# Optimization experiments

Measured on AMD Instinct MI355X. Metric: run time of the kernel, lower is better.

## Reference

```python
import jax, jax.numpy as jnp
import numpy as np

E = 1024
H = 16
DH = E // H
EPS = 1e-8
GRAM_W = 1.5


def _gram_scores(q, k1, k2):
    # q: [BH, L, D], k1/k2: [BH, S, D] -> [BH, L, S]
    ll = jnp.sum(q * q, -1)[:, :, None]          # [BH, L, 1]
    vv = jnp.sum(k1 * k1, -1)[:, None, :]        # [BH, 1, S]
    aa = jnp.sum(k2 * k2, -1)[:, None, :]
    va = jnp.sum(k1 * k2, -1)[:, None, :]
    lv = jnp.einsum('bld,bsd->bls', q, k1)
    la = jnp.einsum('bld,bsd->bls', q, k2)
    det = ll * (vv * aa - va * va) - lv * (lv * aa - la * va) + la * (lv * va - la * vv)
    return -jnp.sqrt(jnp.clip(det, EPS, None))


def setup_inputs() -> dict:
    key = jax.random.key(0)
    ks = jax.random.split(key, 20)
    L, B, S = 512, 4, 1024
    inp = {
        'query': jax.random.normal(ks[0], (L, B, E), jnp.float32),
        'mod1': jax.random.normal(ks[1], (S, B, E), jnp.float32),
        'mod2': jax.random.normal(ks[2], (S, B, E), jnp.float32),
    }
    # Linear params stored as [in, out] (y = x @ W + b), 8 linears
    names = ['q', 'k1', 'k2', 'v1', 'v2', 'g1', 'g2', 'o']
    for i, n in enumerate(names):
        inp[n + '_w'] = jax.random.normal(ks[3 + 2 * i], (E, E), jnp.float32) * 0.02
        inp[n + '_b'] = jax.random.normal(ks[4 + 2 * i], (E,), jnp.float32) * 0.02
    return inp


def reference(query, mod1, mod2,
              q_w, q_b, k1_w, k1_b, k2_w, k2_b, v1_w, v1_b, v2_w, v2_b,
              g1_w, g1_b, g2_w, g2_b, o_w, o_b):
    L, B, _ = query.shape
    S = mod1.shape[0]
    scaling = DH ** -0.5

    def lin(x, w, b):
        return x @ w + b

    def split_heads(x, n):  # [n, B, E] -> [B*H, n, DH]
        return x.reshape(n, B * H, DH).transpose(1, 0, 2)

    q = split_heads(lin(query, q_w, q_b) * scaling, L)
    k1 = split_heads(lin(mod1, k1_w, k1_b), S)
    k2 = split_heads(lin(mod2, k2_w, k2_b), S)
    v1 = split_heads(lin(mod1, v1_w, v1_b), S)
    v2 = split_heads(lin(mod2, v2_w, v2_b), S)

    w1 = jnp.einsum('bld,bsd->bls', q, k1)
    w2 = jnp.einsum('bld,bsd->bls', q, k2)
    gram = _gram_scores(q, k1, k2)
    logits = GRAM_W * gram + w1 + w2          # [BH, L, S]
    attn = jax.nn.softmax(logits, axis=-1)

    def merge_heads(x):  # [B*H, L, DH] -> [L, B, E]
        return x.transpose(1, 0, 2).reshape(L, B, E)

    out1 = merge_heads(jnp.einsum('bls,bsd->bld', attn, v1))
    out2 = merge_heads(jnp.einsum('bls,bsd->bld', attn, v2))
    gate1 = jax.nn.sigmoid(lin(query, g1_w, g1_b))
    gate2 = jax.nn.sigmoid(lin(query, g2_w, g2_b))
    attn_output = lin((out1 * gate1 + out2 * gate2) / 2.0, o_w, o_b)
    avg_weights = attn.reshape(B, H, L, S).mean(axis=1)
    return attn_output, avg_weights
```

## Files before the change

### kernel.cpp

```cpp
#include <hip/hip_runtime.h>
#include <cstddef>
#include <cstdint>

typedef unsigned short ushort_t;
typedef unsigned int uint_t;
typedef __attribute__((ext_vector_type(8))) short short8;
typedef __attribute__((ext_vector_type(4))) float f32x4;

#define EDIM 1024
#define NHEAD 16
#define HDIM 64
#define NB 4
#define LQ 512
#define SK 1024
#define BHD 64

__device__ __forceinline__ ushort_t f2b(float f) {
    uint_t u = __float_as_uint(f);
    return (ushort_t)((u + 0x7fffu + ((u >> 16) & 1u)) >> 16);
}
__device__ __forceinline__ float b2f(ushort_t b) {
    return __uint_as_float(((uint_t)b) << 16);
}

__device__ __forceinline__ void gload_lds16(const void* g, void* l) {
    __builtin_amdgcn_global_load_lds((const __attribute__((address_space(1))) void*)g,
                                     (__attribute__((address_space(3))) void*)l, 16, 0, 0);
}

struct MegaArgs {
    const ushort_t *qx, *m1h, *m1l, *m2h, *m2l;
    const ushort_t *Wqg, *Wkv1, *Wkv2, *Wk1l, *Wk2l;
    const float *q_b, *k1_b, *k2_b, *v1_b, *v2_b, *g1_b, *g2_b;
    float *K1f, *K2f;
    ushort_t *V1b, *V2b, *Qb, *G1b, *G2b;
};

__global__ __launch_bounds__(256, 2)
void mega_gemm(MegaArgs a)
{
    __shared__ ushort_t As[128 * 64];
    __shared__ ushort_t Bs[128 * 64];
    const int tid = threadIdx.x;
    const int wave = tid >> 6, lane = tid & 63;
    const int ln = lane & 15, lq = lane >> 4;
    const int wm = wave & 1, wn = wave >> 1;
    const int cswz = (lane & 7) ^ ((lane >> 3) & 7);
    const int mrl = lane >> 3;

    const int id = blockIdx.x;
    const ushort_t *A, *Al, *B, *Bl;
    const float* bias;
    int npass, row0, col0, kind;
    if (id < 512) {
        kind = id >> 8;
        const int t = id & 255;
        col0 = (t & 7) * 128; row0 = (t >> 3) * 128; npass = 3;
        A = kind ? a.m2h : a.m1h;  Al = kind ? a.m2l : a.m1l;
        B = kind ? a.Wkv2 : a.Wkv1; Bl = kind ? a.Wk2l : a.Wk1l;
        bias = kind ? a.k2_b : a.k1_b;
    } else if (id < 1024) {
        int t = id - 512; kind = 2 + (t >> 8); t &= 255;
        col0 = (t & 7) * 128; row0 = (t >> 3) * 128; npass = 1;
        A = (kind == 2) ? a.m1h : a.m2h; Al = A;
        B = ((kind == 2) ? a.Wkv1 : a.Wkv2) + (size_t)1024 * 1024; Bl = B;
        bias = (kind == 2) ? a.v1_b : a.v2_b;
    } else {
        const int t = id - 1024; kind = 4;
        const int c = t % 24, rr = t / 24;
        col0 = c * 128; row0 = rr * 128; npass = 1;
        A = a.qx; Al = A; B = a.Wqg; Bl = B;
        const int seg = c >> 3;
        bias = (seg == 0) ? a.q_b : ((seg == 1) ? a.g1_b : a.g2_b);
    }

    f32x4 zero = {0.f, 0.f, 0.f, 0.f};
    f32x4 acc[4][4];
#pragma unroll
    for (int i = 0; i < 4; ++i)
#pragma unroll
        for (int j = 0; j < 4; ++j) acc[i][j] = zero;

    for (int pp = 0; pp < npass; ++pp) {
        const ushort_t* Ab = (pp == 2) ? Al : A;
        const ushort_t* Bb = (pp == 1) ? Bl : B;
        for (int kk = 0; kk < 1024; kk += 64) {
            __syncthreads();
#pragma unroll
            for (int j = 0; j < 4; ++j) {
                const int mr = (wave * 4 + j) * 8 + mrl;
                gload_lds16(Ab + (size_t)(row0 + mr) * 1024 + kk + cswz * 8,
                            (void*)(As + (wave * 4 + j) * 512));
                gload_lds16(Bb + (size_t)(col0 + mr) * 1024 + kk + cswz * 8,
                            (void*)(Bs + (wave * 4 + j) * 512));
            }
            __syncthreads();
#pragma unroll
            for (int sub = 0; sub < 2; ++sub) {
                short8 af[4], bfv[4];
#pragma unroll
                for (int i = 0; i < 4; ++i) {
                    const int ml = wm * 64 + i * 16 + ln;
                    af[i] = *(const short8*)(As + ml * 64 + (((sub * 4 + lq) ^ (ml & 7)) * 8));
                    const int nl = wn * 64 + i * 16 + ln;
                    bfv[i] = *(const short8*)(Bs + nl * 64 + (((sub * 4 + lq) ^ (nl & 7)) * 8));
                }
#pragma unroll
                for (int i = 0; i < 4; ++i)
#pragma unroll
                    for (int j = 0; j < 4; ++j)
                        acc[i][j] = __builtin_amdgcn_mfma_f32_16x16x32_bf16(af[i], bfv[j], acc[i][j], 0, 0, 0);
            }
        }
    }

#pragma unroll
    for (int i = 0; i < 4; ++i) {
#pragma unroll
        for (int r = 0; r < 4; ++r) {
            const int row = row0 + wm * 64 + i * 16 + lq * 4 + r;
#pragma unroll
            for (int j = 0; j < 4; ++j) {
                const int col = col0 + wn * 64 + j * 16 + ln;
                const int lc = col & 1023;
                float v = acc[i][j][r] + bias[lc];
                if (kind <= 1) {
                    const int s = row >> 2, b = row & 3, h = lc >> 6, d = lc & 63;
                    float* Y = kind ? a.K2f : a.K1f;
                    Y[(((size_t)(b * 16 + h)) * 1024 + s) * 64 + d] = v;
                } else if (kind <= 3) {
                    const int s = row >> 2, b = row & 3, h = lc >> 6, d = lc & 63;
                    ushort_t* Y = (kind == 2) ? a.V1b : a.V2b;
                    Y[(((size_t)(b * 16 + h)) * 1024 + s) * 64 + d] = f2b(v);
                } else {
                    const int seg = col >> 10;
                    if (seg == 0) {
                        v *= 0.125f;
                        const int s = row >> 2, b = row & 3, h = lc >> 6, d = lc & 63;
                        a.Qb[(((size_t)(b * 16 + h)) * 512 + s) * 64 + d] = f2b(v);
                    } else {
                        v = 1.0f / (1.0f + __expf(-v));
                        ushort_t* Y = (seg == 1) ? a.G1b : a.G2b;
                        Y[(size_t)row * 1024 + lc] = f2b(v);
                    }
                }
            }
        }
    }
}

struct CastArgs {
    const float* q; const float* m1; const float* m2;
    ushort_t* qx; ushort_t* m1h; ushort_t* m1l; ushort_t* m2h; ushort_t* m2l;
    const float* wsrc[8];
    ushort_t* whi[8];
    ushort_t* wlo[8];
};

__global__ __launch_bounds__(256)
void casts_kernel(CastArgs a)
{
    __shared__ float T[64][65];
    const int id = blockIdx.x;
    const int tid = threadIdx.x;
    if (id < 1024) {
        const size_t i = ((size_t)id * 256 + tid) * 8;
        float4 x = *(const float4*)(a.q + i);
        float4 y = *(const float4*)(a.q + i + 4);
        ushort_t o[8] = {f2b(x.x), f2b(x.y), f2b(x.z), f2b(x.w), f2b(y.x), f2b(y.y), f2b(y.z), f2b(y.w)};
        *(uint4*)( (void*)(a.qx + i) ) = *(const uint4*)o;
    } else if (id < 5120) {
        const int t = id - 1024;
        const int which = t >> 11;
        const float* x = which ? a.m2 : a.m1;
        ushort_t* yh = which ? a.m2h : a.m1h;
        ushort_t* yl = which ? a.m2l : a.m1l;
        const size_t i = ((size_t)(t & 2047) * 256 + tid) * 8;
        float v[8];
        *(float4*)v = *(const float4*)(x + i);
        *(float4*)(v + 4) = *(const float4*)(x + i + 4);
        ushort_t oh[8], ol[8];
#pragma unroll
        for (int k = 0; k < 8; ++k) {
            oh[k] = f2b(v[k]);
            ol[k] = f2b(v[k] - b2f(oh[k]));
        }
        *(uint4*)( (void*)(yh + i) ) = *(const uint4*)oh;
        *(uint4*)( (void*)(yl + i) ) = *(const uint4*)ol;
    } else {
        const int t = id - 5120;
        const int z = t >> 8, x = t & 15, y = (t >> 4) & 15;
        const float* W = a.wsrc[z];
        ushort_t* Th = a.whi[z];
        ushort_t* Tl = a.wlo[z];
        const int k0 = x * 64, n0 = y * 64;
        const int r = tid >> 2, cg = (tid & 3) * 16;
#pragma unroll
        for (int u = 0; u < 4; ++u) {
            float4 v = *(const float4*)(W + (size_t)(k0 + r) * 1024 + n0 + cg + u * 4);
            T[r][cg + u * 4 + 0] = v.x; T[r][cg + u * 4 + 1] = v.y;
            T[r][cg + u * 4 + 2] = v.z; T[r][cg + u * 4 + 3] = v.w;
        }
        __syncthreads();
        ushort_t oh[16], ol[16];
#pragma unroll
        for (int u = 0; u < 16; ++u) {
            float v = T[cg + u][r];
            oh[u] = f2b(v);
            ol[u] = f2b(v - b2f(oh[u]));
        }
        ushort_t* dh = Th + (size_t)(n0 + r) * 1024 + k0 + cg;
        *(uint4*)( (void*)dh ) = *(const uint4*)oh;
        *(uint4*)( (void*)(dh + 8) ) = *(const uint4*)(oh + 8);
        if (Tl) {
            ushort_t* dl = Tl + (size_t)(n0 + r) * 1024 + k0 + cg;
            *(uint4*)( (void*)dl ) = *(const uint4*)ol;
            *(uint4*)( (void*)(dl + 8) ) = *(const uint4*)(ol + 8);
        }
    }
}

__global__ __launch_bounds__(256)
void prep_kernel(const float* __restrict__ K1f, const float* __restrict__ K2f,
                 ushort_t* __restrict__ K1b, ushort_t* __restrict__ K2b,
                 float* __restrict__ vv, float* __restrict__ aa, float* __restrict__ va,
                 const ushort_t* __restrict__ Qb, float* __restrict__ ll,
                 const ushort_t* __restrict__ V1b, const ushort_t* __restrict__ V2b,
                 ushort_t* __restrict__ V1t, ushort_t* __restrict__ V2t)
{
    __shared__ float T[64][65];
    const int id = blockIdx.x;
    const int tid = threadIdx.x;
    const int wave = tid >> 6, lane = tid & 63;
    if (id < 16384) {
        const int row = id * 4 + wave;
        const float x1 = K1f[(size_t)row * 64 + lane];
        const float x2 = K2f[(size_t)row * 64 + lane];
        K1b[(size_t)row * 64 + lane] = f2b(x1);
        K2b[(size_t)row * 64 + lane] = f2b(x2);
        float s1 = x1 * x1, s2 = x2 * x2, s3 = x1 * x2;
#pragma unroll
        for (int o = 1; o < 64; o <<= 1) {
            s1 += __shfl_xor(s1, o);
            s2 += __shfl_xor(s2, o);
            s3 += __shfl_xor(s3, o);
        }
        if (lane == 0) { vv[row] = s1; aa[row] = s2; va[row] = s3; }
    } else if (id < 24576) {
        const int row = (id - 16384) * 4 + wave;
        const float x = b2f(Qb[(size_t)row * 64 + lane]);
        float s = x * x;
#pragma unroll
        for (int o = 1; o < 64; o <<= 1) s += __shfl_xor(s, o);
        if (lane == 0) ll[row] = s;
    } else {
        const int t = id - 24576;
        const int z = t >> 10, bh = (t >> 4) & 63, s0 = (t & 15) * 64;
        const ushort_t* S = z ? V2b : V1b;
        ushort_t* D = z ? V2t : V1t;
        const int r = tid >> 2, cg = (tid & 3) * 16;
        ushort_t buf[16];
        const ushort_t* sp = S + ((size_t)bh * 1024 + s0 + r) * 64 + cg;
        *(uint4*)buf = *(const uint4*)sp;
        *(uint4*)(buf + 8) = *(const uint4*)(sp + 8);
#pragma unroll
        for (int u = 0; u < 16; ++u) T[r][cg + u] = b2f(buf[u]);
        __syncthreads();
        ushort_t o[16];
#pragma unroll
        for (int u = 0; u < 16; ++u) o[u] = f2b(T[cg + u][r]);
        ushort_t* d = D + ((size_t)bh * 64 + r) * 1024 + s0 + cg;
        *(uint4*)( (void*)d ) = *(const uint4*)o;
        *(uint4*)( (void*)(d + 8) ) = *(const uint4*)(o + 8);
    }
}

__global__ __launch_bounds__(256, 2)
void scores_kernel(const ushort_t* __restrict__ Qb, const ushort_t* __restrict__ K1b,
                   const ushort_t* __restrict__ K2b, const float* __restrict__ ll,
                   const float* __restrict__ vv, const float* __restrict__ aa,
                   const float* __restrict__ va, float* __restrict__ logits)
{
    __shared__ ushort_t Qs[128 * 64];
    __shared__ ushort_t K1s[128 * 64];
    __shared__ ushort_t K2s[128 * 64];
    __shared__ float llS[128], vvS[128], aaS[128], vaS[128];
    const int tid = threadIdx.x;
    const int wave = tid >> 6, lane = tid & 63;
    const int ln = lane & 15, lq = lane >> 4;
    const int wm = wave & 1, wn = wave >> 1;
    const int bh = blockIdx.z;
    const int l0 = blockIdx.y * 128, s0 = blockIdx.x * 128;
    const int cswz = (lane & 7) ^ ((lane >> 3) & 7);
    const int mrl = lane >> 3;

    if (tid < 128) {
        llS[tid] = ll[(size_t)bh * 512 + l0 + tid];
        vvS[tid] = vv[(size_t)bh * 1024 + s0 + tid];
        aaS[tid] = aa[(size_t)bh * 1024 + s0 + tid];
        vaS[tid] = va[(size_t)bh * 1024 + s0 + tid];
    }
#pragma unroll
    for (int j = 0; j < 4; ++j) {
        const int mr = (wave * 4 + j) * 8 + mrl;
        gload_lds16(Qb + ((size_t)bh * 512 + l0 + mr) * 64 + cswz * 8, (void*)(Qs + (wave * 4 + j) * 512));
        gload_lds16(K1b + ((size_t)bh * 1024 + s0 + mr) * 64 + cswz * 8, (void*)(K1s + (wave * 4 + j) * 512));
        gload_lds16(K2b + ((size_t)bh * 1024 + s0 + mr) * 64 + cswz * 8, (void*)(K2s + (wave * 4 + j) * 512));
    }
    __syncthreads();

    f32x4 zero = {0.f, 0.f, 0.f, 0.f};
    f32x4 lv[4][4], la[4][4];
#pragma unroll
    for (int i = 0; i < 4; ++i)
#pragma unroll
        for (int j = 0; j < 4; ++j) { lv[i][j] = zero; la[i][j] = zero; }

#pragma unroll
    for (int sub = 0; sub < 2; ++sub) {
        short8 qf[4], k1f[4], k2f[4];
#pragma unroll
        for (int i = 0; i < 4; ++i) {
            const int ml = wm * 64 + i * 16 + ln;
            qf[i] = *(const short8*)(Qs + ml * 64 + (((sub * 4 + lq) ^ (ml & 7)) * 8));
            const int nl = wn * 64 + i * 16 + ln;
            k1f[i] = *(const short8*)(K1s + nl * 64 + (((sub * 4 + lq) ^ (nl & 7)) * 8));
            k2f[i] = *(const short8*)(K2s + nl * 64 + (((sub * 4 + lq) ^ (nl & 7)) * 8));
        }
#pragma unroll
        for (int i = 0; i < 4; ++i)
#pragma unroll
            for (int j = 0; j < 4; ++j) {
                lv[i][j] = __builtin_amdgcn_mfma_f32_16x16x32_bf16(qf[i], k1f[j], lv[i][j], 0, 0, 0);
                la[i][j] = __builtin_amdgcn_mfma_f32_16x16x32_bf16(qf[i], k2f[j], la[i][j], 0, 0, 0);
            }
    }

#pragma unroll
    for (int i = 0; i < 4; ++i) {
#pragma unroll
        for (int r = 0; r < 4; ++r) {
            const int l_loc = wm * 64 + i * 16 + lq * 4 + r;
            const float LL = llS[l_loc];
#pragma unroll
            for (int j = 0; j < 4; ++j) {
                const int s_loc = wn * 64 + j * 16 + ln;
                const float VV = vvS[s_loc], AA = aaS[s_loc], VA = vaS[s_loc];
                const float LV = lv[i][j][r], LA = la[i][j][r];
                float det = LL * (VV * AA - VA * VA) - LV * (LV * AA - LA * VA) + LA * (LV * VA - LA * VV);
                det = fmaxf(det, 1e-8f);
                logits[((size_t)bh * 512 + l0 + l_loc) * 1024 + s0 + s_loc] = LV + LA - 1.5f * sqrtf(det);
            }
        }
    }
}

__global__ __launch_bounds__(256)
void softmax_avg_kernel(float* __restrict__ logits, float* __restrict__ avg)
{
    __shared__ float part[4][1024];
    const int b = blockIdx.x >> 9, l = blockIdx.x & 511;
    const int wave = threadIdx.x >> 6, lane = threadIdx.x & 63;
    float pacc[16];
#pragma unroll
    for (int u = 0; u < 16; ++u) pacc[u] = 0.f;
#pragma unroll
    for (int jj = 0; jj < 4; ++jj) {
        const int h = wave * 4 + jj;
        float* rowp = logits + (((size_t)(b * 16 + h)) * 512 + l) * 1024;
        float4 v[4];
#pragma unroll
        for (int c = 0; c < 4; ++c) v[c] = *(const float4*)(rowp + c * 256 + lane * 4);
        float m = -3.4e38f;
#pragma unroll
        for (int c = 0; c < 4; ++c) m = fmaxf(m, fmaxf(fmaxf(v[c].x, v[c].y), fmaxf(v[c].z, v[c].w)));
#pragma unroll
        for (int o = 1; o < 64; o <<= 1) m = fmaxf(m, __shfl_xor(m, o));
        float s = 0.f;
#pragma unroll
        for (int c = 0; c < 4; ++c) {
            v[c].x = __expf(v[c].x - m); v[c].y = __expf(v[c].y - m);
            v[c].z = __expf(v[c].z - m); v[c].w = __expf(v[c].w - m);
            s += v[c].x + v[c].y + v[c].z + v[c].w;
        }
#pragma unroll
        for (int o = 1; o < 64; o <<= 1) s += __shfl_xor(s, o);
        const float inv = 1.0f / s;
        ushort_t* arow = (ushort_t*)rowp;
#pragma unroll
        for (int c = 0; c < 4; ++c) {
            const float p0 = v[c].x * inv, p1 = v[c].y * inv, p2 = v[c].z * inv, p3 = v[c].w * inv;
            ushort_t w[4] = {f2b(p0), f2b(p1), f2b(p2), f2b(p3)};
            *(uint2*)( (void*)(arow + c * 256 + lane * 4) ) = *(const uint2*)w;
            pacc[c * 4 + 0] += p0; pacc[c * 4 + 1] += p1;
            pacc[c * 4 + 2] += p2; pacc[c * 4 + 3] += p3;
        }
    }
#pragma unroll
    for (int c = 0; c < 4; ++c) {
        float4 pv = {pacc[c * 4 + 0], pacc[c * 4 + 1], pacc[c * 4 + 2], pacc[c * 4 + 3]};
        *(float4*)(&part[wave][c * 256 + lane * 4]) = pv;
    }
    __syncthreads();
    const int s0 = threadIdx.x * 4;
    float4 a0 = *(const float4*)(&part[0][s0]);
    float4 a1 = *(const float4*)(&part[1][s0]);
    float4 a2 = *(const float4*)(&part[2][s0]);
    float4 a3 = *(const float4*)(&part[3][s0]);
    float4 o;
    o.x = (a0.x + a1.x + a2.x + a3.x) * 0.0625f;
    o.y = (a0.y + a1.y + a2.y + a3.y) * 0.0625f;
    o.z = (a0.z + a1.z + a2.z + a3.z) * 0.0625f;
    o.w = (a0.w + a1.w + a2.w + a3.w) * 0.0625f;
    *(float4*)(avg + ((size_t)(b * 512 + l)) * 1024 + s0) = o;
}

__global__ __launch_bounds__(256, 2)
void pv_gate_kernel(const ushort_t* __restrict__ attn, const ushort_t* __restrict__ V1t,
                    const ushort_t* __restrict__ V2t, const ushort_t* __restrict__ G1,
                    const ushort_t* __restrict__ G2, ushort_t* __restrict__ tmpb)
{
    __shared__ ushort_t Ps[128 * 64];
    __shared__ ushort_t V1s[64 * 64];
    __shared__ ushort_t V2s[64 * 64];
    const int tid = threadIdx.x;
    const int wave = tid >> 6, lane = tid & 63;
    const int ln = lane & 15, lq = lane >> 4;
    const int bh = blockIdx.y;
    const int l0 = blockIdx.x * 128;
    const int cswz = (lane & 7) ^ ((lane >> 3) & 7);
    const int mrl = lane >> 3;
    const int bq = bh >> 4, h = bh & 15;

    f32x4 zero = {0.f, 0.f, 0.f, 0.f};
    f32x4 acc1[2][4], acc2[2][4];
#pragma unroll
    for (int i = 0; i < 2; ++i)
#pragma unroll
        for (int j = 0; j < 4; ++j) { acc1[i][j] = zero; acc2[i][j] = zero; }

    for (int s0 = 0; s0 < 1024; s0 += 64) {
        __syncthreads();
#pragma unroll
        for (int j = 0; j < 4; ++j) {
            const int mr = (wave * 4 + j) * 8 + mrl;
            gload_lds16(attn + ((size_t)bh * 512 + l0 + mr) * 2048 + s0 + cswz * 8,
                        (void*)(Ps + (wave * 4 + j) * 512));
        }
#pragma unroll
        for (int j = 0; j < 2; ++j) {
            const int mv = (wave * 2 + j) * 8 + mrl;
            gload_lds16(V1t + ((size_t)bh * 64 + mv) * 1024 + s0 + cswz * 8,
                        (void*)(V1s + (wave * 2 + j) * 512));
            gload_lds16(V2t + ((size_t)bh * 64 + mv) * 1024 + s0 + cswz * 8,
                        (void*)(V2s + (wave * 2 + j) * 512));
        }
        __syncthreads();
#pragma unroll
        for (int sub = 0; sub < 2; ++sub) {
            short8 af[2], b1f[4], b2f_[4];
#pragma unroll
            for (int i = 0; i < 2; ++i) {
                const int ml = wave * 32 + i * 16 + ln;
                af[i] = *(const short8*)(Ps + ml * 64 + (((sub * 4 + lq) ^ (ml & 7)) * 8));
            }
#pragma unroll
            for (int j = 0; j < 4; ++j) {
                const int nl = j * 16 + ln;
                b1f[j] = *(const short8*)(V1s + nl * 64 + (((sub * 4 + lq) ^ (nl & 7)) * 8));
                b2f_[j] = *(const short8*)(V2s + nl * 64 + (((sub * 4 + lq) ^ (nl & 7)) * 8));
            }
#pragma unroll
            for (int i = 0; i < 2; ++i)
#pragma unroll
                for (int j = 0; j < 4; ++j) {
                    acc1[i][j] = __builtin_amdgcn_mfma_f32_16x16x32_bf16(af[i], b1f[j], acc1[i][j], 0, 0, 0);
                    acc2[i][j] = __builtin_amdgcn_mfma_f32_16x16x32_bf16(af[i], b2f_[j], acc2[i][j], 0, 0, 0);
                }
        }
    }

#pragma unroll
    for (int i = 0; i < 2; ++i) {
#pragma unroll
        for (int r = 0; r < 4; ++r) {
            const int l = l0 + wave * 32 + i * 16 + lq * 4 + r;
#pragma unroll
            for (int j = 0; j < 4; ++j) {
                const int d = j * 16 + ln;
                const size_t addr = ((size_t)l * 4 + bq) * 1024 + h * 64 + d;
                const float v = 0.5f * (acc1[i][j][r] * b2f(G1[addr]) + acc2[i][j][r] * b2f(G2[addr]));
                tmpb[addr] = f2b(v);
            }
        }
    }
}

__global__ __launch_bounds__(256, 2)
void gemm_o64(const ushort_t* __restrict__ A, const ushort_t* __restrict__ B,
              const float* __restrict__ bias, float* __restrict__ Y)
{
    __shared__ ushort_t As[64 * 64];
    __shared__ ushort_t Bs[128 * 64];
    const int tid = threadIdx.x;
    const int wave = tid >> 6, lane = tid & 63;
    const int ln = lane & 15, lq = lane >> 4;
    const int row0 = blockIdx.y * 64, col0 = blockIdx.x * 128;
    const int wm = wave & 1, wn = wave >> 1;
    const int cswz = (lane & 7) ^ ((lane >> 3) & 7);
    const int mrl = lane >> 3;

    f32x4 zero = {0.f, 0.f, 0.f, 0.f};
    f32x4 acc[2][4];
#pragma unroll
    for (int i = 0; i < 2; ++i)
#pragma unroll
        for (int j = 0; j < 4; ++j) acc[i][j] = zero;

    for (int kk = 0; kk < 1024; kk += 64) {
        __syncthreads();
#pragma unroll
        for (int j = 0; j < 2; ++j) {
            const int mr = (wave * 2 + j) * 8 + mrl;
            gload_lds16(A + (size_t)(row0 + mr) * 1024 + kk + cswz * 8,
                        (void*)(As + (wave * 2 + j) * 512));
        }
#pragma unroll
        for (int j = 0; j < 4; ++j) {
            const int mr = (wave * 4 + j) * 8 + mrl;
            gload_lds16(B + (size_t)(col0 + mr) * 1024 + kk + cswz * 8,
                        (void*)(Bs + (wave * 4 + j) * 512));
        }
        __syncthreads();
#pragma unroll
        for (int sub = 0; sub < 2; ++sub) {
            short8 af[2], bfv[4];
#pragma unroll
            for (int i = 0; i < 2; ++i) {
                const int ml = wm * 32 + i * 16 + ln;
                af[i] = *(const short8*)(As + ml * 64 + (((sub * 4 + lq) ^ (ml & 7)) * 8));
            }
#pragma unroll
            for (int j = 0; j < 4; ++j) {
                const int nl = wn * 64 + j * 16 + ln;
                bfv[j] = *(const short8*)(Bs + nl * 64 + (((sub * 4 + lq) ^ (nl & 7)) * 8));
            }
#pragma unroll
            for (int i = 0; i < 2; ++i)
#pragma unroll
                for (int j = 0; j < 4; ++j)
                    acc[i][j] = __builtin_amdgcn_mfma_f32_16x16x32_bf16(af[i], bfv[j], acc[i][j], 0, 0, 0);
        }
    }

#pragma unroll
    for (int i = 0; i < 2; ++i) {
#pragma unroll
        for (int r = 0; r < 4; ++r) {
            const int row = row0 + wm * 32 + i * 16 + lq * 4 + r;
#pragma unroll
            for (int j = 0; j < 4; ++j) {
                const int col = col0 + wn * 64 + j * 16 + ln;
                Y[(size_t)row * 1024 + col] = acc[i][j][r] + bias[col];
            }
        }
    }
}

extern "C" void kernel_launch(void* const* d_in, const int* in_sizes, int n_in,
                              void* d_out, int out_size, void* d_ws, size_t ws_size,
                              hipStream_t stream)
{
    const float* query = (const float*)d_in[0];
    const float* mod1  = (const float*)d_in[1];
    const float* mod2  = (const float*)d_in[2];
    const float* q_w  = (const float*)d_in[3];  const float* q_b  = (const float*)d_in[4];
    const float* k1_w = (const float*)d_in[5];  const float* k1_b = (const float*)d_in[6];
    const float* k2_w = (const float*)d_in[7];  const float* k2_b = (const float*)d_in[8];
    const float* v1_w = (const float*)d_in[9];  const float* v1_b = (const float*)d_in[10];
    const float* v2_w = (const float*)d_in[11]; const float* v2_b = (const float*)d_in[12];
    const float* g1_w = (const float*)d_in[13]; const float* g1_b = (const float*)d_in[14];
    const float* g2_w = (const float*)d_in[15]; const float* g2_b = (const float*)d_in[16];
    const float* o_w  = (const float*)d_in[17]; const float* o_b  = (const float*)d_in[18];
    float* out = (float*)d_out;

    const size_t MB = 1u << 20;
    char* w = (char*)d_ws;
    ushort_t* Wqg  = (ushort_t*)(w + 0 * MB);
    ushort_t* Wkv1 = (ushort_t*)(w + 6 * MB);
    ushort_t* Wkv2 = (ushort_t*)(w + 10 * MB);
    ushort_t* Wo   = (ushort_t*)(w + 14 * MB);
    ushort_t* Wk1l = (ushort_t*)(w + 16 * MB);
    ushort_t* Wk2l = (ushort_t*)(w + 18 * MB);
    ushort_t* qx   = (ushort_t*)(w + 20 * MB);
    ushort_t* tmpb = qx;
    ushort_t* Qb   = (ushort_t*)(w + 24 * MB);
    ushort_t* K1b  = (ushort_t*)(w + 28 * MB);
    ushort_t* K2b  = (ushort_t*)(w + 36 * MB);
    ushort_t* V1t  = (ushort_t*)(w + 44 * MB);
    ushort_t* V2t  = (ushort_t*)(w + 52 * MB);
    ushort_t* G1b  = (ushort_t*)(w + 60 * MB);
    ushort_t* G2b  = (ushort_t*)(w + 64 * MB);
    float* ll = (float*)(w + 68 * MB);
    float* vv = (float*)(w + 68 * MB + 256 * 1024);
    float* aa = (float*)(w + 68 * MB + 512 * 1024);
    float* va = (float*)(w + 68 * MB + 768 * 1024);
    float* logits = (float*)(w + 78 * MB);
    ushort_t* m1h = (ushort_t*)(w + 78 * MB);
    ushort_t* m2h = (ushort_t*)(w + 86 * MB);
    ushort_t* m1l = (ushort_t*)(w + 94 * MB);
    ushort_t* m2l = (ushort_t*)(w + 102 * MB);
    float* K1f = (float*)(w + 110 * MB);
    float* K2f = (float*)(w + 126 * MB);
    ushort_t* V1b = (ushort_t*)(w + 142 * MB);
    ushort_t* V2b = (ushort_t*)(w + 150 * MB);
    ushort_t* attn = (ushort_t*)logits;

    CastArgs ca;
    ca.q = query; ca.m1 = mod1; ca.m2 = mod2;
    ca.qx = qx; ca.m1h = m1h; ca.m1l = m1l; ca.m2h = m2h; ca.m2l = m2l;
    const float* srcs[8] = {q_w, g1_w, g2_w, k1_w, v1_w, k2_w, v2_w, o_w};
    ushort_t* his[8] = {Wqg, Wqg + (size_t)1024 * 1024, Wqg + (size_t)2048 * 1024,
                        Wkv1, Wkv1 + (size_t)1024 * 1024, Wkv2, Wkv2 + (size_t)1024 * 1024, Wo};
    ushort_t* los[8] = {nullptr, nullptr, nullptr, Wk1l, nullptr, Wk2l, nullptr, nullptr};
    for (int i = 0; i < 8; ++i) { ca.wsrc[i] = srcs[i]; ca.whi[i] = his[i]; ca.wlo[i] = los[i]; }
    casts_kernel<<<7168, 256, 0, stream>>>(ca);

    MegaArgs ma;
    ma.qx = qx; ma.m1h = m1h; ma.m1l = m1l; ma.m2h = m2h; ma.m2l = m2l;
    ma.Wqg = Wqg; ma.Wkv1 = Wkv1; ma.Wkv2 = Wkv2; ma.Wk1l = Wk1l; ma.Wk2l = Wk2l;
    ma.q_b = q_b; ma.k1_b = k1_b; ma.k2_b = k2_b; ma.v1_b = v1_b; ma.v2_b = v2_b;
    ma.g1_b = g1_b; ma.g2_b = g2_b;
    ma.K1f = K1f; ma.K2f = K2f; ma.V1b = V1b; ma.V2b = V2b;
    ma.Qb = Qb; ma.G1b = G1b; ma.G2b = G2b;
    mega_gemm<<<1408, 256, 0, stream>>>(ma);

    prep_kernel<<<26624, 256, 0, stream>>>(K1f, K2f, K1b, K2b, vv, aa, va,
                                           Qb, ll, V1b, V2b, V1t, V2t);

    scores_kernel<<<dim3(8, 4, 64), 256, 0, stream>>>(Qb, K1b, K2b, ll, vv, aa, va, logits);
    softmax_avg_kernel<<<2048, 256, 0, stream>>>(logits, out + (size_t)LQ * NB * EDIM);
    pv_gate_kernel<<<dim3(4, 64), 256, 0, stream>>>(attn, V1t, V2t, G1b, G2b, tmpb);
    gemm_o64<<<dim3(8, 32), 256, 0, stream>>>(tmpb, Wo, o_b, out);
}
```

Baseline: 390.3 us.

## Fuse split-bf16 K GEMM passes into one k-loop and remap block tile order

The K1/K2 projection blocks previously ran three full k-passes (hi*hi, hi*lo, lo*hi), reloading A and B tiles each time. Now each 32-wide k-step loads hi and lo halves together into shared memory and issues all three MFMA groups from one load, cutting barrier count and redundant global traffic. Block-to-tile mapping for all GEMM kinds is also reordered so neighbouring blocks share weight columns, for better L2 reuse. This costs more registers for the extra fragments, which may affect occupancy under launch_bounds(256,2).

```diff
diff --git a/kernel.cpp b/kernel.cpp
--- a/kernel.cpp
+++ b/kernel.cpp
@@ -45,72 +45,146 @@
     const int wave = tid >> 6, lane = tid & 63;
     const int ln = lane & 15, lq = lane >> 4;
     const int wm = wave & 1, wn = wave >> 1;
-    const int cswz = (lane & 7) ^ ((lane >> 3) & 7);
     const int mrl = lane >> 3;
+    const int lswz = (lane & 7) ^ mrl;
 
     const int id = blockIdx.x;
-    const ushort_t *A, *Al, *B, *Bl;
+    f32x4 zero = {0.f, 0.f, 0.f, 0.f};
+
+    if (id < 512) {
+        const int kind = id >> 8;
+        const int t = id & 255;
+        const int u = t >> 3;
+        const int col0 = (u >> 2) * 128;
+        const int row0 = ((t & 7) * 4 + (u & 3)) * 128;
+        const ushort_t* Ah  = kind ? a.m2h : a.m1h;
+        const ushort_t* Alo = kind ? a.m2l : a.m1l;
+        const ushort_t* Bh  = kind ? a.Wkv2 : a.Wkv1;
+        const ushort_t* Blo = kind ? a.Wk2l : a.Wk1l;
+        const float* bias = kind ? a.k2_b : a.k1_b;
+
+        f32x4 acc[4][4];
+#pragma unroll
+        for (int i = 0; i < 4; ++i)
+#pragma unroll
+            for (int j = 0; j < 4; ++j) acc[i][j] = zero;
+
+        const int ksub = (lswz & 3) * 8;
+        const ushort_t* Asrc = (lswz & 4) ? Alo : Ah;
+        const ushort_t* Bsrc = (lswz & 4) ? Blo : Bh;
+
+        for (int kk = 0; kk < 1024; kk += 32) {
+            __syncthreads();
+#pragma unroll
+            for (int j = 0; j < 4; ++j) {
+                const int mr = (wave * 4 + j) * 8 + mrl;
+                gload_lds16(Asrc + (size_t)(row0 + mr) * 1024 + kk + ksub,
+                            (void*)(As + (wave * 4 + j) * 512));
+                gload_lds16(Bsrc + (size_t)(col0 + mr) * 1024 + kk + ksub,
+                            (void*)(Bs + (wave * 4 + j) * 512));
+            }
+            __syncthreads();
+            short8 ah[4], alv[4], bh[4], blv[4];
+#pragma unroll
+            for (int i = 0; i < 4; ++i) {
+                const int ml = wm * 64 + i * 16 + ln;
+                const int pa = (lq ^ (ml & 7)) * 8;
+                ah[i]  = *(const short8*)(As + ml * 64 + pa);
+                alv[i] = *(const short8*)(As + ml * 64 + (pa ^ 32));
+                const int nl = wn * 64 + i * 16 + ln;
+                const int pb = (lq ^ (nl & 7)) * 8;
+                bh[i]  = *(const short8*)(Bs + nl * 64 + pb);
+                blv[i] = *(const short8*)(Bs + nl * 64 + (pb ^ 32));
+            }
+#pragma unroll
+            for (int i = 0; i < 4; ++i)
+#pragma unroll
+                for (int j = 0; j < 4; ++j)
+                    acc[i][j] = __builtin_amdgcn_mfma_f32_16x16x32_bf16(ah[i], bh[j], acc[i][j], 0, 0, 0);
+#pragma unroll
+            for (int i = 0; i < 4; ++i)
+#pragma unroll
+                for (int j = 0; j < 4; ++j)
+                    acc[i][j] = __builtin_amdgcn_mfma_f32_16x16x32_bf16(ah[i], blv[j], acc[i][j], 0, 0, 0);
+#pragma unroll
+            for (int i = 0; i < 4; ++i)
+#pragma unroll
+                for (int j = 0; j < 4; ++j)
+                    acc[i][j] = __builtin_amdgcn_mfma_f32_16x16x32_bf16(alv[i], bh[j], acc[i][j], 0, 0, 0);
+        }
+
+        float* Y = kind ? a.K2f : a.K1f;
+#pragma unroll
+        for (int i = 0; i < 4; ++i) {
+#pragma unroll
+            for (int r = 0; r < 4; ++r) {
+                const int row = row0 + wm * 64 + i * 16 + lq * 4 + r;
+#pragma unroll
+                for (int j = 0; j < 4; ++j) {
+                    const int col = col0 + wn * 64 + j * 16 + ln;
+                    const float v = acc[i][j][r] + bias[col];
+                    const int s = row >> 2, b = row & 3, h = col >> 6, d = col & 63;
+                    Y[(((size_t)(b * 16 + h)) * 1024 + s) * 64 + d] = v;
+                }
+            }
+        }
+        return;
+    }
+
+    int kind, row0, col0;
+    const ushort_t *A, *B;
     const float* bias;
-    int npass, row0, col0, kind;
-    if (id < 512) {
-        kind = id >> 8;
-        const int t = id & 255;
-        col0 = (t & 7) * 128; row0 = (t >> 3) * 128; npass = 3;
-        A = kind ? a.m2h : a.m1h;  Al = kind ? a.m2l : a.m1l;
-        B = kind ? a.Wkv2 : a.Wkv1; Bl = kind ? a.Wk2l : a.Wk1l;
-        bias = kind ? a.k2_b : a.k1_b;
-    } else if (id < 1024) {
+    if (id < 1024) {
         int t = id - 512; kind = 2 + (t >> 8); t &= 255;
-        col0 = (t & 7) * 128; row0 = (t >> 3) * 128; npass = 1;
-        A = (kind == 2) ? a.m1h : a.m2h; Al = A;
-        B = ((kind == 2) ? a.Wkv1 : a.Wkv2) + (size_t)1024 * 1024; Bl = B;
+        const int u = t >> 3;
+        col0 = (u >> 2) * 128;
+        row0 = ((t & 7) * 4 + (u & 3)) * 128;
+        A = (kind == 2) ? a.m1h : a.m2h;
+        B = ((kind == 2) ? a.Wkv1 : a.Wkv2) + (size_t)1024 * 1024;
         bias = (kind == 2) ? a.v1_b : a.v2_b;
     } else {
         const int t = id - 1024; kind = 4;
-        const int c = t % 24, rr = t / 24;
-        col0 = c * 128; row0 = rr * 128; npass = 1;
-        A = a.qx; Al = A; B = a.Wqg; Bl = B;
+        const int u = t >> 3;
+        const int c = (t & 7) * 3 + (u >> 4);
+        const int rr = u & 15;
+        col0 = c * 128; row0 = rr * 128;
+        A = a.qx; B = a.Wqg;
         const int seg = c >> 3;
         bias = (seg == 0) ? a.q_b : ((seg == 1) ? a.g1_b : a.g2_b);
     }
 
-    f32x4 zero = {0.f, 0.f, 0.f, 0.f};
     f32x4 acc[4][4];
 #pragma unroll
     for (int i = 0; i < 4; ++i)
 #pragma unroll
         for (int j = 0; j < 4; ++j) acc[i][j] = zero;
 
-    for (int pp = 0; pp < npass; ++pp) {
-        const ushort_t* Ab = (pp == 2) ? Al : A;
-        const ushort_t* Bb = (pp == 1) ? Bl : B;
-        for (int kk = 0; kk < 1024; kk += 64) {
-            __syncthreads();
-#pragma unroll
-            for (int j = 0; j < 4; ++j) {
-                const int mr = (wave * 4 + j) * 8 + mrl;
-                gload_lds16(Ab + (size_t)(row0 + mr) * 1024 + kk + cswz * 8,
-                            (void*)(As + (wave * 4 + j) * 512));
-                gload_lds16(Bb + (size_t)(col0 + mr) * 1024 + kk + cswz * 8,
-                            (void*)(Bs + (wave * 4 + j) * 512));
-            }
-            __syncthreads();
-#pragma unroll
-            for (int sub = 0; sub < 2; ++sub) {
-                short8 af[4], bfv[4];
-#pragma unroll
-                for (int i = 0; i < 4; ++i) {
-                    const int ml = wm * 64 + i * 16 + ln;
-                    af[i] = *(const short8*)(As + ml * 64 + (((sub * 4 + lq) ^ (ml & 7)) * 8));
-                    const int nl = wn * 64 + i * 16 + ln;
-                    bfv[i] = *(const short8*)(Bs + nl * 64 + (((sub * 4 + lq) ^ (nl & 7)) * 8));
-                }
-#pragma unroll
-                for (int i = 0; i < 4; ++i)
-#pragma unroll
-                    for (int j = 0; j < 4; ++j)
-                        acc[i][j] = __builtin_amdgcn_mfma_f32_16x16x32_bf16(af[i], bfv[j], acc[i][j], 0, 0, 0);
-            }
+    for (int kk = 0; kk < 1024; kk += 64) {
+        __syncthreads();
+#pragma unroll
+        for (int j = 0; j < 4; ++j) {
+            const int mr = (wave * 4 + j) * 8 + mrl;
+            gload_lds16(A + (size_t)(row0 + mr) * 1024 + kk + lswz * 8,
+                        (void*)(As + (wave * 4 + j) * 512));
+            gload_lds16(B + (size_t)(col0 + mr) * 1024 + kk + lswz * 8,
+                        (void*)(Bs + (wave * 4 + j) * 512));
+        }
+        __syncthreads();
+#pragma unroll
+        for (int sub = 0; sub < 2; ++sub) {
+            short8 af[4], bfv[4];
+#pragma unroll
+            for (int i = 0; i < 4; ++i) {
+                const int ml = wm * 64 + i * 16 + ln;
+                af[i] = *(const short8*)(As + ml * 64 + (((sub * 4 + lq) ^ (ml & 7)) * 8));
+                const int nl = wn * 64 + i * 16 + ln;
+                bfv[i] = *(const short8*)(Bs + nl * 64 + (((sub * 4 + lq) ^ (nl & 7)) * 8));
+            }
+#pragma unroll
+            for (int i = 0; i < 4; ++i)
+#pragma unroll
+                for (int j = 0; j < 4; ++j)
+                    acc[i][j] = __builtin_amdgcn_mfma_f32_16x16x32_bf16(af[i], bfv[j], acc[i][j], 0, 0, 0);
         }
     }
 
@@ -124,11 +198,7 @@
                 const int col = col0 + wn * 64 + j * 16 + ln;
                 const int lc = col & 1023;
                 float v = acc[i][j][r] + bias[lc];
-                if (kind <= 1) {
-                    const int s = row >> 2, b = row & 3, h = lc >> 6, d = lc & 63;
-                    float* Y = kind ? a.K2f : a.K1f;
-                    Y[(((size_t)(b * 16 + h)) * 1024 + s) * 64 + d] = v;
-                } else if (kind <= 3) {
+                if (kind <= 3) {
                     const int s = row >> 2, b = row & 3, h = lc >> 6, d = lc & 63;
                     ushort_t* Y = (kind == 2) ? a.V1b : a.V2b;
                     Y[(((size_t)(b * 16 + h)) * 1024 + s) * 64 + d] = f2b(v);
```

Result: faster. 372.0 us (-4.7%).
